# Performance work log

Measured on AMD Instinct MI355X. Metric: run time of the kernel, lower is better.

Reference implementation:

```python
import jax, jax.numpy as jnp
import numpy as np

PATCH = 3       # patch_size
PAD = PATCH // 2
ITERS = 5       # iterations
RADIUS = 4      # random_search radius


def get_patches(feats, nnf):
    # feats: [b,c,H,W]; nnf: [b,2,h,w] float coords (row, col)
    # Returns per-pixel patches [b,h,w,P,P,c] gathered at rounded, clipped coords
    b, c, H, W = feats.shape
    fp = jnp.pad(feats, ((0, 0), (0, 0), (PAD, PAD), (PAD, PAD)))
    fp = jnp.transpose(fp, (0, 2, 3, 1))  # [b,H+2p,W+2p,c]
    y = jnp.clip(jnp.round(nnf[:, 0]), 0, H - 1).astype(jnp.int32)  # [b,h,w]
    x = jnp.clip(jnp.round(nnf[:, 1]), 0, W - 1).astype(jnp.int32)
    off = jnp.arange(PATCH)
    yy = y[..., None, None] + off[:, None]   # [b,h,w,P,1] (already offset by PAD in padded frame)
    xx = x[..., None, None] + off[None, :]   # [b,h,w,1,P]
    bi = jnp.arange(b)[:, None, None, None, None]
    return fp[bi, yy, xx]  # [b,h,w,P,P,c]


def patch_distance(ps, pt):
    # SSD over patch and channel dims -> [b,h,w]
    return jnp.sum((ps - pt) ** 2, axis=(3, 4, 5))


def propagate(nnf, source, target, direction):
    shifted = jnp.roll(nnf, direction, axis=3)
    cur_d = patch_distance(get_patches(source, nnf), get_patches(target, nnf))
    shf_d = patch_distance(get_patches(source, shifted), get_patches(target, shifted))
    mask = (shf_d < cur_d)[:, None]  # [b,1,h,w]
    return jnp.where(mask, shifted, nnf)


def random_search(nnf, source, target, key):
    hmax = target.shape[2] - 1  # torch code clamps both coords to H-1
    cur_d = patch_distance(get_patches(source, nnf), get_patches(target, nnf))
    for i in range(RADIUS):
        key, k = jax.random.split(key)
        rand_nnf = jnp.clip(
            nnf + jax.random.normal(k, nnf.shape, nnf.dtype) * (2.0 ** (-i)),
            0.0, float(hmax))
        rand_d = patch_distance(get_patches(source, rand_nnf), get_patches(target, rand_nnf))
        mask = rand_d < cur_d  # [b,h,w]
        nnf = jnp.where(mask[:, None], rand_nnf, nnf)
        cur_d = jnp.where(mask, rand_d, cur_d)
    return nnf


def setup_inputs() -> dict:
    key = jax.random.key(0)
    k1, k2 = jax.random.split(key)
    source = jax.random.normal(k1, (2, 32, 256, 256), dtype=jnp.float32)
    target = jax.random.normal(k2, (2, 32, 256, 256), dtype=jnp.float32)
    return {"source": source, "target": target}


def reference(source, target):
    b, c, h, w = source.shape
    k0 = jax.random.key(1)
    k_init, k_loop = jax.random.split(k0)
    # init_nnf: uniform in [0, H_t-1] x [0, W_t-1]
    nnf = jax.random.uniform(k_init, (b, 2, h, w), dtype=source.dtype)
    scale = jnp.array([target.shape[2] - 1, target.shape[3] - 1], source.dtype)
    nnf = nnf * scale[None, :, None, None]
    for t in range(ITERS):
        nnf = propagate(nnf, source, target, 1)
        nnf = propagate(nnf, source, target, -1)
        nnf = random_search(nnf, source, target, jax.random.fold_in(k_loop, t))
    return nnf
```

## Files before the change

### kernel.cpp

```cpp
#include <hip/hip_runtime.h>
#include <stdint.h>

#define DEVFN __device__ __forceinline__

DEVFN float mulf(float a, float b) {
#pragma clang fp contract(off)
  return a * b;
}
DEVFN float addf(float a, float b) {
#pragma clang fp contract(off)
  return a + b;
}
DEVFN float subf(float a, float b) {
#pragma clang fp contract(off)
  return a - b;
}

DEVFN uint32_t tf_bits32(uint32_t k0, uint32_t k1, uint32_t ctr) {
  uint32_t ks2 = k0 ^ k1 ^ 0x1BD11BDAu;
  uint32_t x0 = k0;
  uint32_t x1 = ctr + k1;
#define TFR(d) { x0 += x1; x1 = (x1 << (d)) | (x1 >> (32 - (d))); x1 ^= x0; }
  TFR(13) TFR(15) TFR(26) TFR(6)
  x0 += k1; x1 += ks2 + 1u;
  TFR(17) TFR(29) TFR(16) TFR(24)
  x0 += ks2; x1 += k0 + 2u;
  TFR(13) TFR(15) TFR(26) TFR(6)
  x0 += k0; x1 += k1 + 3u;
  TFR(17) TFR(29) TFR(16) TFR(24)
  x0 += k1; x1 += ks2 + 4u;
  TFR(13) TFR(15) TFR(26) TFR(6)
  x0 += ks2; x1 += k0 + 5u;
#undef TFR
  return x0 ^ x1;
}

DEVFN float xla_cephes_logf(float in) {
  float xv = fmaxf(in, __uint_as_float(0x00800000u));
  uint32_t bits = __float_as_uint(xv);
  int ei = (int)(bits >> 23) - 126;
  float m = __uint_as_float((bits & 0x007FFFFFu) | 0x3F000000u);
  float e = (float)ei;
  const float SQRTHF = __uint_as_float(0x3F3504F3u);
  bool lt = m < SQRTHF;
  float tmp = lt ? m : 0.0f;
  m = subf(m, 1.0f);
  e = subf(e, lt ? 1.0f : 0.0f);
  m = addf(m, tmp);
  float z = mulf(m, m);
  float y = 7.0376836292E-2f;
  y = addf(mulf(y, m), -1.1514610310E-1f);
  y = addf(mulf(y, m),  1.1676998740E-1f);
  y = addf(mulf(y, m), -1.2420140846E-1f);
  y = addf(mulf(y, m),  1.4249322787E-1f);
  y = addf(mulf(y, m), -1.6668057665E-1f);
  y = addf(mulf(y, m),  2.0000714765E-1f);
  y = addf(mulf(y, m), -2.4999993993E-1f);
  y = addf(mulf(y, m),  3.3333331174E-1f);
  y = mulf(y, m);
  y = mulf(y, z);
  y = addf(y, mulf(e, -2.12194440e-4f));
  y = subf(y, mulf(z, 0.5f));
  m = addf(m, y);
  m = addf(m, mulf(e, 0.693359375f));
  return m;
}

DEVFN float xla_log1pf(float a) {
  float large = xla_cephes_logf(addf(a, 1.0f));
  float small = mulf(addf(mulf(-0.5f, a), 1.0f), a);
  return (fabsf(a) < __uint_as_float(0x38D1B717u)) ? small : large;
}

DEVFN float xla_erfinvf(float u) {
  float nxx = -mulf(u, u);
  float w = -xla_log1pf(nxx);
  float p;
  if (w < 5.0f) {
    float s = subf(w, 2.5f);
    p = 2.81022636e-08f;
    p = addf(mulf(p, s), 3.43273939e-07f);
    p = addf(mulf(p, s), -3.5233877e-06f);
    p = addf(mulf(p, s), -4.39150654e-06f);
    p = addf(mulf(p, s), 0.00021858087f);
    p = addf(mulf(p, s), -0.00125372503f);
    p = addf(mulf(p, s), -0.00417768164f);
    p = addf(mulf(p, s), 0.246640727f);
    p = addf(mulf(p, s), 1.50140941f);
  } else {
    float s = subf(__fsqrt_rn(w), 3.0f);
    p = -0.000200214257f;
    p = addf(mulf(p, s), 0.000100950558f);
    p = addf(mulf(p, s), 0.00134934322f);
    p = addf(mulf(p, s), -0.00367342844f);
    p = addf(mulf(p, s), 0.00573950773f);
    p = addf(mulf(p, s), -0.0076224613f);
    p = addf(mulf(p, s), 0.00943887047f);
    p = addf(mulf(p, s), 1.00167406f);
    p = addf(mulf(p, s), 2.83297682f);
  }
  return mulf(p, u);
}

DEVFN float unitf(uint32_t bits) {
  return subf(__uint_as_float((bits >> 9) | 0x3F800000u), 1.0f);
}

DEVFN float jax_normal(uint32_t bits) {
  float f = unitf(bits);
  const float lo = __uint_as_float(0xBF7FFFFFu);
  float u = fmaxf(lo, addf(mulf(f, 2.0f), lo));
  const float sqrt2 = __uint_as_float(0x3FB504F3u);
  return mulf(sqrt2, xla_erfinvf(u));
}

struct PMKeys {
  uint32_t ki0, ki1;
  uint32_t sk[5][4][2];
};
struct NK { uint32_t k[20][2]; };

DEVFN float candf(float base, float n, float sig) {
  return fminf(fmaxf(addf(base, mulf(n, sig)), 0.0f), 255.0f);
}
DEVFN int addr_of(float yy, float xx) {
  int iy = (int)rintf(yy);
  int ix = (int)rintf(xx);
  iy = min(max(iy, 0), 255);
  ix = min(max(ix, 0), 255);
  return iy * 256 + ix;
}


__global__ __launch_bounds__(256) void qdiff_n(const float* __restrict__ S,
                                               const float* __restrict__ T,
                                               float* __restrict__ Q,
                                               float* __restrict__ N,
                                               NK nk) {
  __shared__ float lds[64 * 33];
  const int t = threadIdx.x;
  const int gid = blockIdx.x;
  const int b = gid >> 10;
  const int y = (gid >> 2) & 255;
  const int x0 = (gid & 3) << 6;
  const int xl = t & 63;
  const int cw = t >> 6;

  float sv[8], tv[8];
#pragma unroll
  for (int k = 0; k < 8; ++k) {
    int c = k * 4 + cw;
    size_t o = (size_t)(b * 32 + c) * 65536 + (size_t)y * 256 + x0 + xl;
    sv[k] = S[o];
    tv[k] = T[o];
  }

  uint32_t gtid = (uint32_t)gid * 256u + (uint32_t)t;
#pragma unroll
  for (int i = 0; i < 10; ++i) {
    uint32_t L = (uint32_t)i * 524288u + gtid;
    uint32_t ts = L >> 18;
    uint32_t idx = L & 262143u;
    N[L] = jax_normal(tf_bits32(nk.k[ts][0], nk.k[ts][1], idx));
  }

#pragma unroll
  for (int k = 0; k < 8; ++k) {
    int c = k * 4 + cw;
    float d = subf(sv[k], tv[k]);
    lds[xl * 33 + c] = mulf(d, d);
  }
  __syncthreads();
  size_t base = (size_t)gid * 2048;
#pragma unroll
  for (int k = 0; k < 2; ++k) {
    int e = t * 4 + k * 1024;
    int px = e >> 5, c = e & 31;
    float4 v;
    v.x = lds[px * 33 + c];
    v.y = lds[px * 33 + c + 1];
    v.z = lds[px * 33 + c + 2];
    v.w = lds[px * 33 + c + 3];
    *(float4*)&Q[base + e] = v;
  }
}

__global__ __launch_bounds__(256) void dsum_kernel(const float* __restrict__ Q,
                                                   float* __restrict__ D) {
  const int x = threadIdx.x;
  const int bid = blockIdx.x;
  const int swz = (bid & 7) * 64 + (bid >> 3);
  const int y = swz & 255;
  const int b = swz >> 8;
  float acc = 0.0f;
  for (int py = 0; py < 3; ++py) {
    int yy = y + py - 1;
    if (yy < 0 || yy > 255) continue;
    for (int px = 0; px < 3; ++px) {
      int xx = x + px - 1;
      if (xx < 0 || xx > 255) continue;
      const float4* p = (const float4*)&Q[((size_t)b * 65536 + yy * 256 + xx) * 32];
      float4 v0 = p[0], v1 = p[1], v2 = p[2], v3 = p[3];
      float4 v4 = p[4], v5 = p[5], v6 = p[6], v7 = p[7];
      acc = addf(acc, v0.x); acc = addf(acc, v0.y); acc = addf(acc, v0.z); acc = addf(acc, v0.w);
      acc = addf(acc, v1.x); acc = addf(acc, v1.y); acc = addf(acc, v1.z); acc = addf(acc, v1.w);
      acc = addf(acc, v2.x); acc = addf(acc, v2.y); acc = addf(acc, v2.z); acc = addf(acc, v2.w);
      acc = addf(acc, v3.x); acc = addf(acc, v3.y); acc = addf(acc, v3.z); acc = addf(acc, v3.w);
      acc = addf(acc, v4.x); acc = addf(acc, v4.y); acc = addf(acc, v4.z); acc = addf(acc, v4.w);
      acc = addf(acc, v5.x); acc = addf(acc, v5.y); acc = addf(acc, v5.z); acc = addf(acc, v5.w);
      acc = addf(acc, v6.x); acc = addf(acc, v6.y); acc = addf(acc, v6.z); acc = addf(acc, v6.w);
      acc = addf(acc, v7.x); acc = addf(acc, v7.y); acc = addf(acc, v7.z); acc = addf(acc, v7.w);
    }
  }
  D[(b * 256 + y) * 256 + x] = acc;
}

__global__ __launch_bounds__(256) void pm_fast(const float* __restrict__ D,
                                               const float* __restrict__ N,
                                               float* __restrict__ out,
                                               uint32_t ki0, uint32_t ki1) {
  const int j = threadIdx.x;
  const int bb = blockIdx.x >> 8;
  const int i = blockIdx.x & 255;
  const float* Db = D + bb * 65536;
  __shared__ float sy[256], sx[256];

  const uint32_t idx_y = (uint32_t)(bb * 131072 + i * 256 + j);
  const uint32_t idx_x = idx_y + 65536u;

  float nyv[20], nxv[20];
#pragma unroll
  for (int ts = 0; ts < 20; ++ts) {
    nyv[ts] = N[(size_t)ts * 262144 + idx_y];
    nxv[ts] = N[(size_t)ts * 262144 + idx_x];
  }

  float y = mulf(unitf(tf_bits32(ki0, ki1, idx_y)), 255.0f);
  float x = mulf(unitf(tf_bits32(ki0, ki1, idx_x)), 255.0f);

  float curd = Db[addr_of(y, x)];
#pragma unroll
  for (int t = 0; t < 5; ++t) {
    sy[j] = y; sx[j] = x;
    __syncthreads();
    {
      int jn = (j + 255) & 255;
      float yn = sy[jn], xn = sx[jn];
      float shf = Db[addr_of(yn, xn)];
      if (shf < curd) { y = yn; x = xn; curd = shf; }
    }
    __syncthreads();
    sy[j] = y; sx[j] = x;
    __syncthreads();
    {
      int jn = (j + 1) & 255;
      float yn = sy[jn], xn = sx[jn];
      float shf = Db[addr_of(yn, xn)];
      if (shf < curd) { y = yn; x = xn; curd = shf; }
    }
    __syncthreads();

    float n0y = nyv[t * 4 + 0], n0x = nxv[t * 4 + 0];
    float n1y = nyv[t * 4 + 1], n1x = nxv[t * 4 + 1];
    float n2y = nyv[t * 4 + 2], n2x = nxv[t * 4 + 2];
    float n3y = nyv[t * 4 + 3], n3x = nxv[t * 4 + 3];

    float c0y = candf(y, n0y, 1.0f),  c0x = candf(x, n0x, 1.0f);
    float c1Ay = candf(y,   n1y, 0.5f), c1Ax = candf(x,   n1x, 0.5f);
    float c1By = candf(c0y, n1y, 0.5f), c1Bx = candf(c0x, n1x, 0.5f);
    float c2_0y = candf(y,    n2y, 0.25f), c2_0x = candf(x,    n2x, 0.25f);
    float c2_1y = candf(c1Ay, n2y, 0.25f), c2_1x = candf(c1Ax, n2x, 0.25f);
    float c2_2y = candf(c0y,  n2y, 0.25f), c2_2x = candf(c0x,  n2x, 0.25f);
    float c2_3y = candf(c1By, n2y, 0.25f), c2_3x = candf(c1Bx, n2x, 0.25f);
    float c3_0y = candf(y,     n3y, 0.125f), c3_0x = candf(x,     n3x, 0.125f);
    float c3_1y = candf(c2_0y, n3y, 0.125f), c3_1x = candf(c2_0x, n3x, 0.125f);
    float c3_2y = candf(c1Ay,  n3y, 0.125f), c3_2x = candf(c1Ax,  n3x, 0.125f);
    float c3_3y = candf(c2_1y, n3y, 0.125f), c3_3x = candf(c2_1x, n3x, 0.125f);
    float c3_4y = candf(c0y,   n3y, 0.125f), c3_4x = candf(c0x,   n3x, 0.125f);
    float c3_5y = candf(c2_2y, n3y, 0.125f), c3_5x = candf(c2_2x, n3x, 0.125f);
    float c3_6y = candf(c1By,  n3y, 0.125f), c3_6x = candf(c1Bx,  n3x, 0.125f);
    float c3_7y = candf(c2_3y, n3y, 0.125f), c3_7x = candf(c2_3x, n3x, 0.125f);

    float d0   = Db[addr_of(c0y,  c0x)];
    float d1A  = Db[addr_of(c1Ay, c1Ax)];
    float d1B  = Db[addr_of(c1By, c1Bx)];
    float d2_0 = Db[addr_of(c2_0y, c2_0x)];
    float d2_1 = Db[addr_of(c2_1y, c2_1x)];
    float d2_2 = Db[addr_of(c2_2y, c2_2x)];
    float d2_3 = Db[addr_of(c2_3y, c2_3x)];
    float d3_0 = Db[addr_of(c3_0y, c3_0x)];
    float d3_1 = Db[addr_of(c3_1y, c3_1x)];
    float d3_2 = Db[addr_of(c3_2y, c3_2x)];
    float d3_3 = Db[addr_of(c3_3y, c3_3x)];
    float d3_4 = Db[addr_of(c3_4y, c3_4x)];
    float d3_5 = Db[addr_of(c3_5y, c3_5x)];
    float d3_6 = Db[addr_of(c3_6y, c3_6x)];
    float d3_7 = Db[addr_of(c3_7y, c3_7x)];

    bool a0 = d0 < curd;
    y = a0 ? c0y : y;  x = a0 ? c0x : x;  curd = a0 ? d0 : curd;

    float s1y = a0 ? c1By : c1Ay, s1x = a0 ? c1Bx : c1Ax, s1d = a0 ? d1B : d1A;
    bool a1 = s1d < curd;
    y = a1 ? s1y : y;  x = a1 ? s1x : x;  curd = a1 ? s1d : curd;

    float s2y = a0 ? (a1 ? c2_3y : c2_2y) : (a1 ? c2_1y : c2_0y);
    float s2x = a0 ? (a1 ? c2_3x : c2_2x) : (a1 ? c2_1x : c2_0x);
    float s2d = a0 ? (a1 ? d2_3 : d2_2) : (a1 ? d2_1 : d2_0);
    bool a2 = s2d < curd;
    y = a2 ? s2y : y;  x = a2 ? s2x : x;  curd = a2 ? s2d : curd;

    float s3y = a0 ? (a1 ? (a2 ? c3_7y : c3_6y) : (a2 ? c3_5y : c3_4y))
                   : (a1 ? (a2 ? c3_3y : c3_2y) : (a2 ? c3_1y : c3_0y));
    float s3x = a0 ? (a1 ? (a2 ? c3_7x : c3_6x) : (a2 ? c3_5x : c3_4x))
                   : (a1 ? (a2 ? c3_3x : c3_2x) : (a2 ? c3_1x : c3_0x));
    float s3d = a0 ? (a1 ? (a2 ? d3_7 : d3_6) : (a2 ? d3_5 : d3_4))
                   : (a1 ? (a2 ? d3_3 : d3_2) : (a2 ? d3_1 : d3_0));
    bool a3 = s3d < curd;
    y = a3 ? s3y : y;  x = a3 ? s3x : x;  curd = a3 ? s3d : curd;
  }
  out[idx_y] = y;
  out[idx_x] = x;
}


__global__ __launch_bounds__(256) void compute_d(const float* __restrict__ S,
                                                 const float* __restrict__ T,
                                                 float* __restrict__ D) {
  const int x = threadIdx.x;
  const int y = blockIdx.x & 255;
  const int b = blockIdx.x >> 8;
  const int chs = 65536;
  const float* Sb = S + (size_t)b * 32 * chs;
  const float* Tb = T + (size_t)b * 32 * chs;
  float acc = 0.0f;
  for (int py = 0; py < 3; ++py) {
    int yy = y + py - 1;
    if (yy < 0 || yy > 255) continue;
    for (int px = 0; px < 3; ++px) {
      int xx = x + px - 1;
      if (xx < 0 || xx > 255) continue;
      int off = yy * 256 + xx;
      for (int c = 0; c < 32; ++c) {
        float d = subf(Sb[c * chs + off], Tb[c * chs + off]);
        acc = addf(acc, mulf(d, d));
      }
    }
  }
  D[b * chs + y * 256 + x] = acc;
}

__global__ __launch_bounds__(256) void pm_kernel(const float* __restrict__ D,
                                                 float* __restrict__ out,
                                                 PMKeys K) {
  const int j = threadIdx.x;
  const int bb = blockIdx.x >> 8;
  const int i = blockIdx.x & 255;
  const float* Db = D + bb * 65536;
  __shared__ float sy[256], sx[256];

  const uint32_t idx_y = (uint32_t)(bb * 131072 + i * 256 + j);
  const uint32_t idx_x = idx_y + 65536u;

  float y = mulf(unitf(tf_bits32(K.ki0, K.ki1, idx_y)), 255.0f);
  float x = mulf(unitf(tf_bits32(K.ki0, K.ki1, idx_x)), 255.0f);

  auto lookup = [&](float yy, float xx) -> float {
    int iy = (int)rintf(yy);
    int ix = (int)rintf(xx);
    iy = min(max(iy, 0), 255);
    ix = min(max(ix, 0), 255);
    return Db[iy * 256 + ix];
  };

  for (int t = 0; t < 5; ++t) {
    sy[j] = y; sx[j] = x;
    __syncthreads();
    {
      int jn = (j + 255) & 255;
      float yn = sy[jn], xn = sx[jn];
      float cur = lookup(y, x);
      float shf = lookup(yn, xn);
      if (shf < cur) { y = yn; x = xn; }
    }
    __syncthreads();
    sy[j] = y; sx[j] = x;
    __syncthreads();
    {
      int jn = (j + 1) & 255;
      float yn = sy[jn], xn = sx[jn];
      float cur = lookup(y, x);
      float shf = lookup(yn, xn);
      if (shf < cur) { y = yn; x = xn; }
    }
    __syncthreads();
    float cur = lookup(y, x);
    float sigma = 1.0f;
    for (int s = 0; s < 4; ++s) {
      uint32_t kk0 = K.sk[t][s][0], kk1 = K.sk[t][s][1];
      float ny = jax_normal(tf_bits32(kk0, kk1, idx_y));
      float nx = jax_normal(tf_bits32(kk0, kk1, idx_x));
      float ry = fminf(fmaxf(addf(y, mulf(ny, sigma)), 0.0f), 255.0f);
      float rx = fminf(fmaxf(addf(x, mulf(nx, sigma)), 0.0f), 255.0f);
      float rd = lookup(ry, rx);
      if (rd < cur) { y = ry; x = rx; cur = rd; }
      sigma *= 0.5f;
    }
  }
  out[idx_y] = y;
  out[idx_x] = x;
}

static void h_tf(uint32_t k0, uint32_t k1, uint32_t x0, uint32_t x1,
                 uint32_t& o0, uint32_t& o1) {
  uint32_t ks2 = k0 ^ k1 ^ 0x1BD11BDAu;
  x0 += k0; x1 += k1;
#define HR(d) { x0 += x1; x1 = (x1 << (d)) | (x1 >> (32 - (d))); x1 ^= x0; }
  HR(13) HR(15) HR(26) HR(6)
  x0 += k1; x1 += ks2 + 1u;
  HR(17) HR(29) HR(16) HR(24)
  x0 += ks2; x1 += k0 + 2u;
  HR(13) HR(15) HR(26) HR(6)
  x0 += k0; x1 += k1 + 3u;
  HR(17) HR(29) HR(16) HR(24)
  x0 += k1; x1 += ks2 + 4u;
  HR(13) HR(15) HR(26) HR(6)
  x0 += ks2; x1 += k0 + 5u;
#undef HR
  o0 = x0; o1 = x1;
}

extern "C" void kernel_launch(void* const* d_in, const int* in_sizes, int n_in,
                              void* d_out, int out_size, void* d_ws, size_t ws_size,
                              hipStream_t stream) {
  const float* S = (const float*)d_in[0];
  const float* T = (const float*)d_in[1];
  float* out = (float*)d_out;

  PMKeys K;
  uint32_t kl0, kl1;
  h_tf(0u, 1u, 0u, 0u, K.ki0, K.ki1);
  h_tf(0u, 1u, 0u, 1u, kl0, kl1);
  for (uint32_t t = 0; t < 5; ++t) {
    uint32_t c0, c1;
    h_tf(kl0, kl1, 0u, t, c0, c1);
    for (int s = 0; s < 4; ++s) {
      uint32_t n0, n1, s0, s1;
      h_tf(c0, c1, 0u, 0u, n0, n1);
      h_tf(c0, c1, 0u, 1u, s0, s1);
      K.sk[t][s][0] = s0; K.sk[t][s][1] = s1;
      c0 = n0; c1 = n1;
    }
  }

  const size_t D_BYTES = 2ull * 65536 * 4;
  const size_t Q_BYTES = 2ull * 65536 * 32 * 4;
  const size_t N_BYTES = 20ull * 262144 * 4;
  const size_t NEED = D_BYTES + Q_BYTES + N_BYTES;

  if (ws_size >= NEED) {
    float* Dd = (float*)d_ws;
    float* Qq = (float*)((char*)d_ws + D_BYTES);
    float* Nn = (float*)((char*)d_ws + D_BYTES + Q_BYTES);
    NK nk;
    for (int t = 0; t < 5; ++t)
      for (int s = 0; s < 4; ++s) {
        nk.k[t * 4 + s][0] = K.sk[t][s][0];
        nk.k[t * 4 + s][1] = K.sk[t][s][1];
      }
    hipLaunchKernelGGL(qdiff_n, dim3(2048), dim3(256), 0, stream, S, T, Qq, Nn, nk);
    hipLaunchKernelGGL(dsum_kernel, dim3(512), dim3(256), 0, stream, Qq, Dd);
    hipLaunchKernelGGL(pm_fast, dim3(512), dim3(256), 0, stream, Dd, Nn, out, K.ki0, K.ki1);
  } else {
    float* Dd = (float*)d_ws;
    hipLaunchKernelGGL(compute_d, dim3(512), dim3(256), 0, stream, S, T, Dd);
    hipLaunchKernelGGL(pm_kernel, dim3(512), dim3(256), 0, stream, Dd, out, K);
  }
}
```

Measured before the change: 127.4 us.

## Fuse squared-difference and patch-sum kernels, dropping the Q intermediate buffer

```diff
diff --git a/kernel.cpp b/kernel.cpp
--- a/kernel.cpp
+++ b/kernel.cpp
@@ -132,87 +132,70 @@
 }
 
 
-__global__ __launch_bounds__(256) void qdiff_n(const float* __restrict__ S,
-                                               const float* __restrict__ T,
-                                               float* __restrict__ Q,
-                                               float* __restrict__ N,
-                                               NK nk) {
-  __shared__ float lds[64 * 33];
-  const int t = threadIdx.x;
-  const int gid = blockIdx.x;
-  const int b = gid >> 10;
-  const int y = (gid >> 2) & 255;
-  const int x0 = (gid & 3) << 6;
-  const int xl = t & 63;
-  const int cw = t >> 6;
-
-  float sv[8], tv[8];
-#pragma unroll
-  for (int k = 0; k < 8; ++k) {
-    int c = k * 4 + cw;
-    size_t o = (size_t)(b * 32 + c) * 65536 + (size_t)y * 256 + x0 + xl;
-    sv[k] = S[o];
-    tv[k] = T[o];
-  }
-
-  uint32_t gtid = (uint32_t)gid * 256u + (uint32_t)t;
-#pragma unroll
-  for (int i = 0; i < 10; ++i) {
-    uint32_t L = (uint32_t)i * 524288u + gtid;
-    uint32_t ts = L >> 18;
-    uint32_t idx = L & 262143u;
-    N[L] = jax_normal(tf_bits32(nk.k[ts][0], nk.k[ts][1], idx));
-  }
-
-#pragma unroll
-  for (int k = 0; k < 8; ++k) {
-    int c = k * 4 + cw;
-    float d = subf(sv[k], tv[k]);
-    lds[xl * 33 + c] = mulf(d, d);
-  }
-  __syncthreads();
-  size_t base = (size_t)gid * 2048;
-#pragma unroll
-  for (int k = 0; k < 2; ++k) {
-    int e = t * 4 + k * 1024;
-    int px = e >> 5, c = e & 31;
-    float4 v;
-    v.x = lds[px * 33 + c];
-    v.y = lds[px * 33 + c + 1];
-    v.z = lds[px * 33 + c + 2];
-    v.w = lds[px * 33 + c + 3];
-    *(float4*)&Q[base + e] = v;
-  }
-}
-
-__global__ __launch_bounds__(256) void dsum_kernel(const float* __restrict__ Q,
-                                                   float* __restrict__ D) {
-  const int x = threadIdx.x;
+__global__ __launch_bounds__(256) void dn_fused(const float* __restrict__ S,
+                                                const float* __restrict__ T,
+                                                float* __restrict__ D,
+                                                float* __restrict__ N,
+                                                NK nk) {
+  __shared__ float lds[258 * 33];
+  const int tid = threadIdx.x;
   const int bid = blockIdx.x;
+
+  if (bid >= 512) {
+    uint32_t g = (uint32_t)(bid - 512) * 256u + (uint32_t)tid;
+#pragma unroll
+    for (int i = 0; i < 10; ++i) {
+      uint32_t L = (uint32_t)i * 524288u + g;
+      uint32_t ts = L >> 18;
+      uint32_t idx = L & 262143u;
+      N[L] = jax_normal(tf_bits32(nk.k[ts][0], nk.k[ts][1], idx));
+    }
+    return;
+  }
+
   const int swz = (bid & 7) * 64 + (bid >> 3);
   const int y = swz & 255;
   const int b = swz >> 8;
+  const size_t base_b = (size_t)b * 32 * 65536;
+
   float acc = 0.0f;
   for (int py = 0; py < 3; ++py) {
     int yy = y + py - 1;
-    if (yy < 0 || yy > 255) continue;
-    for (int px = 0; px < 3; ++px) {
-      int xx = x + px - 1;
-      if (xx < 0 || xx > 255) continue;
-      const float4* p = (const float4*)&Q[((size_t)b * 65536 + yy * 256 + xx) * 32];
-      float4 v0 = p[0], v1 = p[1], v2 = p[2], v3 = p[3];
-      float4 v4 = p[4], v5 = p[5], v6 = p[6], v7 = p[7];
-      acc = addf(acc, v0.x); acc = addf(acc, v0.y); acc = addf(acc, v0.z); acc = addf(acc, v0.w);
-      acc = addf(acc, v1.x); acc = addf(acc, v1.y); acc = addf(acc, v1.z); acc = addf(acc, v1.w);
-      acc = addf(acc, v2.x); acc = addf(acc, v2.y); acc = addf(acc, v2.z); acc = addf(acc, v2.w);
-      acc = addf(acc, v3.x); acc = addf(acc, v3.y); acc = addf(acc, v3.z); acc = addf(acc, v3.w);
-      acc = addf(acc, v4.x); acc = addf(acc, v4.y); acc = addf(acc, v4.z); acc = addf(acc, v4.w);
-      acc = addf(acc, v5.x); acc = addf(acc, v5.y); acc = addf(acc, v5.z); acc = addf(acc, v5.w);
-      acc = addf(acc, v6.x); acc = addf(acc, v6.y); acc = addf(acc, v6.z); acc = addf(acc, v6.w);
-      acc = addf(acc, v7.x); acc = addf(acc, v7.y); acc = addf(acc, v7.z); acc = addf(acc, v7.w);
-    }
-  }
-  D[(b * 256 + y) * 256 + x] = acc;
+    bool row_ok = (yy >= 0 && yy <= 255);
+    if (row_ok) {
+      const size_t row_off = base_b + (size_t)yy * 256;
+#pragma unroll
+      for (int it = 0; it < 33; ++it) {
+        int e = it * 256 + tid;
+        if (e < 8256) {
+          int c = e / 258;
+          int lx = e - c * 258;
+          int xx = lx - 1;
+          float q = 0.0f;
+          if (xx >= 0 && xx <= 255) {
+            size_t o = row_off + (size_t)c * 65536 + xx;
+            float d = subf(S[o], T[o]);
+            q = mulf(d, d);
+          }
+          lds[lx * 33 + c] = q;
+        }
+      }
+    }
+    __syncthreads();
+    if (row_ok) {
+#pragma unroll
+      for (int px = 0; px < 3; ++px) {
+        int xx = tid + px - 1;
+        if (xx < 0 || xx > 255) continue;
+        const float* p = &lds[(tid + px) * 33];
+#pragma unroll
+        for (int c = 0; c < 32; ++c)
+          acc = addf(acc, p[c]);
+      }
+    }
+    __syncthreads();
+  }
+  D[(b * 256 + y) * 256 + tid] = acc;
 }
 
 __global__ __launch_bounds__(256) void pm_fast(const float* __restrict__ D,
@@ -454,22 +437,19 @@
   }
 
   const size_t D_BYTES = 2ull * 65536 * 4;
-  const size_t Q_BYTES = 2ull * 65536 * 32 * 4;
   const size_t N_BYTES = 20ull * 262144 * 4;
-  const size_t NEED = D_BYTES + Q_BYTES + N_BYTES;
+  const size_t NEED = D_BYTES + N_BYTES;
 
   if (ws_size >= NEED) {
     float* Dd = (float*)d_ws;
-    float* Qq = (float*)((char*)d_ws + D_BYTES);
-    float* Nn = (float*)((char*)d_ws + D_BYTES + Q_BYTES);
+    float* Nn = (float*)((char*)d_ws + D_BYTES);
     NK nk;
     for (int t = 0; t < 5; ++t)
       for (int s = 0; s < 4; ++s) {
         nk.k[t * 4 + s][0] = K.sk[t][s][0];
         nk.k[t * 4 + s][1] = K.sk[t][s][1];
       }
-    hipLaunchKernelGGL(qdiff_n, dim3(2048), dim3(256), 0, stream, S, T, Qq, Nn, nk);
-    hipLaunchKernelGGL(dsum_kernel, dim3(512), dim3(256), 0, stream, Qq, Dd);
+    hipLaunchKernelGGL(dn_fused, dim3(2560), dim3(256), 0, stream, S, T, Dd, Nn, nk);
     hipLaunchKernelGGL(pm_fast, dim3(512), dim3(256), 0, stream, Dd, Nn, out, K.ki0, K.ki1);
   } else {
     float* Dd = (float*)d_ws;
```

Result: no change. 126.3 us (-0.9%).
